# Performance work log

Hardware: AMD Instinct MI355X
Metric: run time of the kernel (lower is better)

## Reference

```python
import jax, jax.numpy as jnp
import numpy as np
import math

B, T, C, H = 8, 1024, 1024, 16
D = C // H  # head dim = 64
EPS = 1e-5


def layernorm(x, g, b):
    mu = jnp.mean(x, axis=-1, keepdims=True)
    var = jnp.var(x, axis=-1, keepdims=True)
    return (x - mu) * jax.lax.rsqrt(var + EPS) * g + b


def setup_inputs() -> dict:
    key = jax.random.key(0)
    ks = jax.random.split(key, 8)
    s = lambda fan_in: 1.0 / math.sqrt(fan_in)
    return {
        "x": jax.random.normal(ks[0], (B, T, C), jnp.float32),
        "Wqkv": jax.random.normal(ks[1], (C, 3 * C), jnp.float32) * s(C),
        "bqkv": jnp.zeros((3 * C,), jnp.float32),
        "Wproj": jax.random.normal(ks[2], (C, C), jnp.float32) * s(C),
        "bproj": jnp.zeros((C,), jnp.float32),
        "ln1_g": jnp.ones((C,), jnp.float32),
        "ln1_b": jnp.zeros((C,), jnp.float32),
        "ln2_g": jnp.ones((C,), jnp.float32),
        "ln2_b": jnp.zeros((C,), jnp.float32),
        "W1": jax.random.normal(ks[3], (C, 4 * C), jnp.float32) * s(C),
        "b1": jnp.zeros((4 * C,), jnp.float32),
        "W2": jax.random.normal(ks[4], (4 * C, C), jnp.float32) * s(4 * C),
        "b2": jnp.zeros((C,), jnp.float32),
    }


def reference(x, Wqkv, bqkv, Wproj, bproj, ln1_g, ln1_b, ln2_g, ln2_b, W1, b1, W2, b2):
    # --- self-attention on ln1(x) ---
    h = layernorm(x, ln1_g, ln1_b)
    qkv = h @ Wqkv + bqkv                          # [B,T,3C]
    q, k, v = jnp.split(qkv, 3, axis=-1)
    # [B,T,C] -> [B,H,T,D]
    q = q.reshape(B, T, H, D).transpose(0, 2, 1, 3)
    k = k.reshape(B, T, H, D).transpose(0, 2, 1, 3)
    v = v.reshape(B, T, H, D).transpose(0, 2, 1, 3)
    # NOTE: original uses 1/sqrt(3*n_embd//n_head), not 1/sqrt(head_dim)
    scale = 1.0 / math.sqrt(3 * C // H)
    attn = jnp.einsum("bhqd,bhkd->bhqk", q, k) * scale  # [B,H,T,T]
    causal = jnp.tril(jnp.ones((T, T), bool))
    attn = jnp.where(causal, attn, -jnp.inf)
    attn = jax.nn.softmax(attn, axis=-1)
    y = jnp.einsum("bhqk,bhkd->bhqd", attn, v)          # [B,H,T,D]
    y = y.transpose(0, 2, 1, 3).reshape(B, T, C)
    x = x + (y @ Wproj + bproj)
    # --- MLP on ln2(x) ---
    h2 = layernorm(x, ln2_g, ln2_b)
    x = x + (jax.nn.relu(h2 @ W1 + b1) @ W2 + b2)
    return x
```

## Files before the change

kernel.cpp:

```cpp
#include <hip/hip_runtime.h>

typedef __bf16 bf16;
typedef __bf16 bf16x8 __attribute__((ext_vector_type(8)));
typedef float f32x4 __attribute__((ext_vector_type(4)));

#define MFMA16(a, b, c) __builtin_amdgcn_mfma_f32_16x16x32_bf16(a, b, c, 0, 0, 0)

static constexpr int Bn = 8;
static constexpr int Tn = 1024;
static constexpr int Cn = 1024;
static constexpr int Hn = 16;

typedef const __attribute__((address_space(1))) unsigned int* gp_t;
typedef __attribute__((address_space(3))) unsigned int* lp_t;
__device__ __forceinline__ void gload_lds16(const bf16* g, bf16* l) {
    __builtin_amdgcn_global_load_lds((gp_t)(const void*)g, (lp_t)(void*)l, 16, 0, 0);
}

__global__ __launch_bounds__(256) void tcast(const float* __restrict__ in,
                                             bf16* __restrict__ out,
                                             int K, int N) {
    __shared__ float tile[32][33];
    const int n0 = blockIdx.x * 32, k0 = blockIdx.y * 32;
    const int tx = threadIdx.x & 31, ty = threadIdx.x >> 5;
#pragma unroll
    for (int i = 0; i < 4; i++)
        tile[ty + 8 * i][tx] = in[(size_t)(k0 + ty + 8 * i) * N + n0 + tx];
    __syncthreads();
#pragma unroll
    for (int i = 0; i < 4; i++)
        out[(size_t)(n0 + ty + 8 * i) * K + k0 + tx] = (bf16)tile[tx][ty + 8 * i];
}

template <typename T>
__global__ __launch_bounds__(256) void ln_row(const T* __restrict__ x,
                                              const float* __restrict__ g,
                                              const float* __restrict__ be,
                                              bf16* __restrict__ out) {
    const int row = blockIdx.x, t = threadIdx.x;
    const T* xr = x + (size_t)row * Cn;
    float v[4], s = 0.f, s2 = 0.f;
#pragma unroll
    for (int i = 0; i < 4; i++) {
        v[i] = (float)xr[t + i * 256];
        s += v[i];
        s2 += v[i] * v[i];
    }
#pragma unroll
    for (int off = 32; off > 0; off >>= 1) {
        s += __shfl_down(s, off);
        s2 += __shfl_down(s2, off);
    }
    __shared__ float red[8];
    const int wave = t >> 6, lane = t & 63;
    if (lane == 0) {
        red[wave] = s;
        red[4 + wave] = s2;
    }
    __syncthreads();
    s = red[0] + red[1] + red[2] + red[3];
    s2 = red[4] + red[5] + red[6] + red[7];
    const float mu = s * (1.f / Cn);
    const float rstd = rsqrtf(s2 * (1.f / Cn) - mu * mu + 1e-5f);
    bf16* orow = out + (size_t)row * Cn;
#pragma unroll
    for (int i = 0; i < 4; i++) {
        int c = t + i * 256;
        orow[c] = (bf16)((v[i] - mu) * rstd * g[c] + be[c]);
    }
}

__global__ __launch_bounds__(256) void vtrans(const bf16* __restrict__ qkv,
                                              bf16* __restrict__ Vt) {
    __shared__ bf16 tile[64 * 72];
    const int tid = threadIdx.x;
    const int bh = blockIdx.x, b = bh >> 4, h = bh & 15;
    const int t0 = blockIdx.y * 64;
    const int r = tid >> 3, c = (tid & 7) * 8;
#pragma unroll
    for (int i = 0; i < 2; i++) {
        const int rr = r + i * 32;
        *(bf16x8*)(tile + rr * 72 + c) =
            *(const bf16x8*)(qkv + ((size_t)(b * Tn + t0 + rr)) * 3072 + 2 * Cn + h * 64 + c);
    }
    __syncthreads();
#pragma unroll
    for (int i = 0; i < 2; i++) {
        const int d = r + i * 32;
        bf16x8 v;
#pragma unroll
        for (int j = 0; j < 8; j++) v[j] = tile[(c + j) * 72 + d];
        *(bf16x8*)(Vt + ((size_t)bh * 64 + d) * Tn + t0 + c) = v;
    }
}

template <int TM, int TN, bool RELU, bool RESID, bool OUTBF16, typename RT>
__global__ __launch_bounds__(256, 2) void gemm_bt(const bf16* __restrict__ A,
                                                  const bf16* __restrict__ Bt,
                                                  const float* __restrict__ bias,
                                                  const RT* __restrict__ resid,
                                                  void* __restrict__ outp,
                                                  int M, int N, int K) {
    constexpr int MI = TM / 32;
    constexpr int NI = TN / 32;
    constexpr int AJ = TM / 32;
    constexpr int BJ = TN / 32;
    __shared__ __align__(16) bf16 As[TM * 64];
    __shared__ __align__(16) bf16 Bs[TN * 64];
    const int t = threadIdx.x;
    const int lane = t & 63, wave = t >> 6;
    const int lane15 = lane & 15, quad = lane >> 4;
    const int m0 = blockIdx.x * TM, n0 = blockIdx.y * TN;
    const int mb = (wave >> 1) * (TM / 2), nb = (wave & 1) * (TN / 2);

    const f32x4 zero4 = {0.f, 0.f, 0.f, 0.f};
    f32x4 acc[MI][NI];
#pragma unroll
    for (int i = 0; i < MI; i++)
#pragma unroll
        for (int j = 0; j < NI; j++) acc[i][j] = zero4;

    const int grow = lane >> 3;
    const int gcol = ((lane & 7) ^ grow) * 8;
    const bf16* gA = A + (size_t)(m0 + wave * (AJ * 8) + grow) * K + gcol;
    const bf16* gB = Bt + (size_t)(n0 + wave * (BJ * 8) + grow) * K + gcol;
    bf16* lA = As + (wave * AJ) * 512;
    bf16* lB = Bs + (wave * BJ) * 512;

    for (int kt = 0; kt < K; kt += 64) {
#pragma unroll
        for (int j = 0; j < AJ; j++)
            gload_lds16(gA + (size_t)(j * 8) * K + kt, lA + j * 512);
#pragma unroll
        for (int j = 0; j < BJ; j++)
            gload_lds16(gB + (size_t)(j * 8) * K + kt, lB + j * 512);
        __syncthreads();
#pragma unroll
        for (int kk = 0; kk < 2; kk++) {
            bf16x8 fa[MI], fb[NI];
#pragma unroll
            for (int mi = 0; mi < MI; mi++) {
                const int r = mb + mi * 16 + lane15;
                fa[mi] = *(const bf16x8*)(As + r * 64 + (((kk * 4 + quad) ^ (r & 7)) * 8));
            }
#pragma unroll
            for (int ni = 0; ni < NI; ni++) {
                const int r = nb + ni * 16 + lane15;
                fb[ni] = *(const bf16x8*)(Bs + r * 64 + (((kk * 4 + quad) ^ (r & 7)) * 8));
            }
#pragma unroll
            for (int mi = 0; mi < MI; mi++)
#pragma unroll
                for (int ni = 0; ni < NI; ni++)
                    acc[mi][ni] = MFMA16(fa[mi], fb[ni], acc[mi][ni]);
        }
        __syncthreads();
    }

    float bsv[NI];
#pragma unroll
    for (int ni = 0; ni < NI; ni++) bsv[ni] = bias[n0 + nb + ni * 16 + lane15];
#pragma unroll
    for (int mi = 0; mi < MI; mi++) {
#pragma unroll
        for (int reg = 0; reg < 4; reg++) {
            const int row = m0 + mb + mi * 16 + quad * 4 + reg;
#pragma unroll
            for (int ni = 0; ni < NI; ni++) {
                const int col = n0 + nb + ni * 16 + lane15;
                float v = acc[mi][ni][reg] + bsv[ni];
                if (RELU) v = v > 0.f ? v : 0.f;
                if (RESID) v += (float)resid[(size_t)row * N + col];
                if (OUTBF16)
                    ((bf16*)outp)[(size_t)row * N + col] = (bf16)v;
                else
                    ((float*)outp)[(size_t)row * N + col] = v;
            }
        }
    }
}

__global__ __launch_bounds__(256) void attn(const bf16* __restrict__ qkv,
                                            const bf16* __restrict__ Vt,
                                            bf16* __restrict__ y) {
    __shared__ __align__(16) bf16 Ks[64 * 72];
    __shared__ __align__(16) bf16 Vs[80 * 72];
    __shared__ __align__(16) bf16 Ps[4][32 * 72];
    const int tid = threadIdx.x, lane = tid & 63, wave = tid >> 6;
    const int lane15 = lane & 15, quad = lane >> 4;
    const int b = blockIdx.x >> 4, h = blockIdx.x & 15;
    const int q0 = blockIdx.y * 128;
    const int qr0 = q0 + wave * 32;
    const float c1 = 0.10412043f;

    for (int i = tid; i < 16 * 72; i += 256)
        Vs[64 * 72 + i] = (bf16)((i < 72) ? 1.0f : 0.0f);

    bf16x8 fq[2][2];
#pragma unroll
    for (int mi = 0; mi < 2; mi++) {
        const size_t qb = ((size_t)(b * Tn + qr0 + mi * 16 + lane15)) * 3072 + h * 64;
#pragma unroll
        for (int kk = 0; kk < 2; kk++)
            fq[mi][kk] = *(const bf16x8*)(qkv + qb + kk * 32 + quad * 8);
    }

    const f32x4 zero4 = {0.f, 0.f, 0.f, 0.f};
    f32x4 o[2][4], lacc[2];
#pragma unroll
    for (int mi = 0; mi < 2; mi++) {
        lacc[mi] = zero4;
#pragma unroll
        for (int ni = 0; ni < 4; ni++) o[mi][ni] = zero4;
    }

    const int sr = tid >> 3, sc = (tid & 7) * 8;
    const int nkb = q0 / 64 + 2;
    for (int kb = 0; kb < nkb; kb++) {
        const int k0 = kb * 64;
#pragma unroll
        for (int i = 0; i < 2; i++) {
            const int r = sr + i * 32;
            *(bf16x8*)(Ks + r * 72 + sc) =
                *(const bf16x8*)(qkv + ((size_t)(b * Tn + k0 + r)) * 3072 + Cn + h * 64 + sc);
            *(bf16x8*)(Vs + r * 72 + sc) =
                *(const bf16x8*)(Vt + ((size_t)blockIdx.x * 64 + r) * Tn + k0 + sc);
        }
        __syncthreads();

        if (k0 <= qr0 + 31) {
            bf16x8 fk[4][2];
#pragma unroll
            for (int ni = 0; ni < 4; ni++)
#pragma unroll
                for (int kk = 0; kk < 2; kk++)
                    fk[ni][kk] = *(const bf16x8*)(Ks + (ni * 16 + lane15) * 72 + kk * 32 + quad * 8);
            f32x4 s[2][4];
#pragma unroll
            for (int mi = 0; mi < 2; mi++)
#pragma unroll
                for (int ni = 0; ni < 4; ni++) {
                    if (k0 + ni * 16 <= qr0 + mi * 16 + 15) {
                        f32x4 a = zero4;
                        a = MFMA16(fq[mi][0], fk[ni][0], a);
                        a = MFMA16(fq[mi][1], fk[ni][1], a);
                        s[mi][ni] = a;
                    }
                }
            const bool domask = (k0 + 63 > qr0);
            if (domask) {
#pragma unroll
                for (int mi = 0; mi < 2; mi++)
#pragma unroll
                    for (int ni = 0; ni < 4; ni++) {
                        bf16* pd = &Ps[wave][(mi * 16 + quad * 4) * 72 + ni * 16 + lane15];
                        if (k0 + ni * 16 > qr0 + mi * 16 + 15) {
#pragma unroll
                            for (int r = 0; r < 4; r++) pd[r * 72] = (bf16)0.f;
                        } else if (k0 + ni * 16 + 15 <= qr0 + mi * 16) {
#pragma unroll
                            for (int r = 0; r < 4; r++)
                                pd[r * 72] = (bf16)__builtin_amdgcn_exp2f(s[mi][ni][r] * c1);
                        } else {
                            const int key = k0 + ni * 16 + lane15;
                            const int row0 = qr0 + mi * 16 + quad * 4;
#pragma unroll
                            for (int r = 0; r < 4; r++) {
                                float L = (key > row0 + r) ? -1e30f : s[mi][ni][r] * c1;
                                pd[r * 72] = (bf16)__builtin_amdgcn_exp2f(L);
                            }
                        }
                    }
            } else {
#pragma unroll
                for (int mi = 0; mi < 2; mi++)
#pragma unroll
                    for (int ni = 0; ni < 4; ni++)
#pragma unroll
                        for (int r = 0; r < 4; r++)
                            Ps[wave][(mi * 16 + quad * 4 + r) * 72 + ni * 16 + lane15] =
                                (bf16)__builtin_amdgcn_exp2f(s[mi][ni][r] * c1);
            }
            bf16x8 fp[2][2];
#pragma unroll
            for (int mi = 0; mi < 2; mi++)
#pragma unroll
                for (int kk = 0; kk < 2; kk++)
                    fp[mi][kk] = *(const bf16x8*)(&Ps[wave][(mi * 16 + lane15) * 72 + kk * 32 + quad * 8]);
            const bool use_kk1 = (k0 + 32 <= qr0 + 31);
#pragma unroll
            for (int ni = 0; ni < 5; ni++) {
                bf16x8 fv0 = *(const bf16x8*)(Vs + (ni * 16 + lane15) * 72 + quad * 8);
                bf16x8 fv1 = *(const bf16x8*)(Vs + (ni * 16 + lane15) * 72 + 32 + quad * 8);
#pragma unroll
                for (int mi = 0; mi < 2; mi++) {
                    f32x4* dst = (ni < 4) ? &o[mi][ni] : &lacc[mi];
                    f32x4 a = *dst;
                    a = MFMA16(fp[mi][0], fv0, a);
                    if (use_kk1) a = MFMA16(fp[mi][1], fv1, a);
                    *dst = a;
                }
            }
        }
        __syncthreads();
    }

#pragma unroll
    for (int mi = 0; mi < 2; mi++)
#pragma unroll
        for (int r = 0; r < 4; r++) {
            float l = __shfl(lacc[mi][r], lane & 48);
            const float inv = 1.f / l;
            const size_t base = ((size_t)(b * Tn + qr0 + mi * 16 + quad * 4 + r)) * Cn + h * 64;
#pragma unroll
            for (int ni = 0; ni < 4; ni++)
                y[base + ni * 16 + lane15] = (bf16)(o[mi][ni][r] * inv);
        }
}

extern "C" void kernel_launch(void* const* d_in, const int* in_sizes, int n_in,
                              void* d_out, int out_size, void* d_ws, size_t ws_size,
                              hipStream_t stream) {
    const float* x = (const float*)d_in[0];
    const float* Wqkv = (const float*)d_in[1];
    const float* bqkv = (const float*)d_in[2];
    const float* Wproj = (const float*)d_in[3];
    const float* bproj = (const float*)d_in[4];
    const float* ln1g = (const float*)d_in[5];
    const float* ln1b = (const float*)d_in[6];
    const float* ln2g = (const float*)d_in[7];
    const float* ln2b = (const float*)d_in[8];
    const float* W1 = (const float*)d_in[9];
    const float* b1 = (const float*)d_in[10];
    const float* W2 = (const float*)d_in[11];
    const float* b2 = (const float*)d_in[12];
    float* out = (float*)d_out;

    char* ws = (char*)d_ws;
    size_t off = 0;
    auto alloc = [&](size_t bytes) {
        void* p = ws + off;
        off += (bytes + 255) & ~(size_t)255;
        return p;
    };
    bf16* WqkvT = (bf16*)alloc((size_t)3072 * 1024 * 2);
    bf16* WprojT = (bf16*)alloc((size_t)1024 * 1024 * 2);
    bf16* W1T = (bf16*)alloc((size_t)4096 * 1024 * 2);
    bf16* W2T = (bf16*)alloc((size_t)1024 * 4096 * 2);
    bf16* hbuf = (bf16*)alloc((size_t)8192 * 1024 * 2);
    bf16* qkvb = (bf16*)alloc((size_t)8192 * 3072 * 2);
    bf16* ybuf = (bf16*)alloc((size_t)8192 * 1024 * 2);
    bf16* vtb = (bf16*)alloc((size_t)8192 * 1024 * 2);
    bf16* x1b = (bf16*)alloc((size_t)8192 * 1024 * 2);
    bf16* a1 = qkvb;

    tcast<<<dim3(3072 / 32, 1024 / 32), 256, 0, stream>>>(Wqkv, WqkvT, 1024, 3072);
    tcast<<<dim3(1024 / 32, 1024 / 32), 256, 0, stream>>>(Wproj, WprojT, 1024, 1024);
    tcast<<<dim3(4096 / 32, 1024 / 32), 256, 0, stream>>>(W1, W1T, 1024, 4096);
    tcast<<<dim3(1024 / 32, 4096 / 32), 256, 0, stream>>>(W2, W2T, 4096, 1024);

    ln_row<float><<<8192, 256, 0, stream>>>(x, ln1g, ln1b, hbuf);
    gemm_bt<128, 256, false, false, true, float><<<dim3(64, 12), 256, 0, stream>>>(
        hbuf, WqkvT, bqkv, (const float*)nullptr, qkvb, 8192, 3072, 1024);
    vtrans<<<dim3(Bn * Hn, Tn / 64), 256, 0, stream>>>(qkvb, vtb);
    attn<<<dim3(Bn * Hn, Tn / 128), 256, 0, stream>>>(qkvb, vtb, ybuf);
    gemm_bt<128, 128, false, true, true, float><<<dim3(64, 8), 256, 0, stream>>>(
        ybuf, WprojT, bproj, x, x1b, 8192, 1024, 1024);
    ln_row<bf16><<<8192, 256, 0, stream>>>(x1b, ln2g, ln2b, hbuf);
    gemm_bt<128, 256, true, false, true, float><<<dim3(64, 16), 256, 0, stream>>>(
        hbuf, W1T, b1, (const float*)nullptr, a1, 8192, 4096, 1024);
    gemm_bt<128, 128, false, true, false, bf16><<<dim3(64, 8), 256, 0, stream>>>(
        a1, W2T, b2, x1b, out, 8192, 1024, 4096);
}
```

Measured before the change: 435.4 us.

## Double-buffer attention K/V via async LDS loads, add BK knob, fuse weight casts

The attention kernel now stages K and V tiles with global_load_lds into double-buffered, XOR-swizzled shared memory. The next block's load is issued before the current block is computed, and the trailing barrier is removed. The P tile also uses the swizzle instead of padding, and the ones-row used for row sums moves to its own buffer. Separately, the GEMM takes a BK template parameter, set to 128 for the two K-heavy N=1024 GEMMs, and the four weight transpose-cast launches are merged into one launch. The intent is to overlap memory with compute and cut launch and barrier overhead. The costs are more LDS, which may lower occupancy, and a possible race on the buffer reuse now that only one barrier remains per iteration.

```diff
diff --git a/kernel.cpp b/kernel.cpp
--- a/kernel.cpp
+++ b/kernel.cpp
@@ -17,11 +17,30 @@
     __builtin_amdgcn_global_load_lds((gp_t)(const void*)g, (lp_t)(void*)l, 16, 0, 0);
 }
 
-__global__ __launch_bounds__(256) void tcast(const float* __restrict__ in,
-                                             bf16* __restrict__ out,
-                                             int K, int N) {
+__global__ __launch_bounds__(256) void tcast_all(const float* __restrict__ Wqkv,
+                                                 const float* __restrict__ Wproj,
+                                                 const float* __restrict__ W1,
+                                                 const float* __restrict__ W2,
+                                                 bf16* __restrict__ WqkvT,
+                                                 bf16* __restrict__ WprojT,
+                                                 bf16* __restrict__ W1T,
+                                                 bf16* __restrict__ W2T) {
+    int bid = blockIdx.x;
+    const float* in;
+    bf16* out;
+    int K, N;
+    if (bid < 3072) {
+        in = Wqkv; out = WqkvT; K = 1024; N = 3072;
+    } else if (bid < 4096) {
+        bid -= 3072; in = Wproj; out = WprojT; K = 1024; N = 1024;
+    } else if (bid < 8192) {
+        bid -= 4096; in = W1; out = W1T; K = 1024; N = 4096;
+    } else {
+        bid -= 8192; in = W2; out = W2T; K = 4096; N = 1024;
+    }
+    const int ntx = N / 32;
+    const int n0 = (bid % ntx) * 32, k0 = (bid / ntx) * 32;
     __shared__ float tile[32][33];
-    const int n0 = blockIdx.x * 32, k0 = blockIdx.y * 32;
     const int tx = threadIdx.x & 31, ty = threadIdx.x >> 5;
 #pragma unroll
     for (int i = 0; i < 4; i++)
@@ -94,7 +113,7 @@
     }
 }
 
-template <int TM, int TN, bool RELU, bool RESID, bool OUTBF16, typename RT>
+template <int TM, int TN, int BK, bool RELU, bool RESID, bool OUTBF16, typename RT>
 __global__ __launch_bounds__(256, 2) void gemm_bt(const bf16* __restrict__ A,
                                                   const bf16* __restrict__ Bt,
                                                   const float* __restrict__ bias,
@@ -103,10 +122,12 @@
                                                   int M, int N, int K) {
     constexpr int MI = TM / 32;
     constexpr int NI = TN / 32;
-    constexpr int AJ = TM / 32;
-    constexpr int BJ = TN / 32;
-    __shared__ __align__(16) bf16 As[TM * 64];
-    __shared__ __align__(16) bf16 Bs[TN * 64];
+    constexpr int CPR = BK / 8;
+    constexpr int RPG = 64 / CPR;
+    constexpr int AJ = TM / (4 * RPG);
+    constexpr int BJ = TN / (4 * RPG);
+    __shared__ __align__(16) bf16 As[TM * BK];
+    __shared__ __align__(16) bf16 Bs[TN * BK];
     const int t = threadIdx.x;
     const int lane = t & 63, wave = t >> 6;
     const int lane15 = lane & 15, quad = lane >> 4;
@@ -120,33 +141,37 @@
 #pragma unroll
         for (int j = 0; j < NI; j++) acc[i][j] = zero4;
 
-    const int grow = lane >> 3;
-    const int gcol = ((lane & 7) ^ grow) * 8;
-    const bf16* gA = A + (size_t)(m0 + wave * (AJ * 8) + grow) * K + gcol;
-    const bf16* gB = Bt + (size_t)(n0 + wave * (BJ * 8) + grow) * K + gcol;
-    bf16* lA = As + (wave * AJ) * 512;
-    bf16* lB = Bs + (wave * BJ) * 512;
-
-    for (int kt = 0; kt < K; kt += 64) {
-#pragma unroll
-        for (int j = 0; j < AJ; j++)
-            gload_lds16(gA + (size_t)(j * 8) * K + kt, lA + j * 512);
-#pragma unroll
-        for (int j = 0; j < BJ; j++)
-            gload_lds16(gB + (size_t)(j * 8) * K + kt, lB + j * 512);
+    const int grow = lane / CPR;
+    const int gsub = lane % CPR;
+
+    for (int kt = 0; kt < K; kt += BK) {
+#pragma unroll
+        for (int j = 0; j < AJ; j++) {
+            const int rj = wave * (AJ * RPG) + j * RPG + grow;
+            const int cj = (gsub ^ (rj & 7)) * 8;
+            gload_lds16(A + (size_t)(m0 + rj) * K + kt + cj,
+                        As + (wave * (AJ * RPG) + j * RPG) * BK);
+        }
+#pragma unroll
+        for (int j = 0; j < BJ; j++) {
+            const int rj = wave * (BJ * RPG) + j * RPG + grow;
+            const int cj = (gsub ^ (rj & 7)) * 8;
+            gload_lds16(Bt + (size_t)(n0 + rj) * K + kt + cj,
+                        Bs + (wave * (BJ * RPG) + j * RPG) * BK);
+        }
         __syncthreads();
 #pragma unroll
-        for (int kk = 0; kk < 2; kk++) {
+        for (int kk = 0; kk < BK / 32; kk++) {
             bf16x8 fa[MI], fb[NI];
 #pragma unroll
             for (int mi = 0; mi < MI; mi++) {
                 const int r = mb + mi * 16 + lane15;
-                fa[mi] = *(const bf16x8*)(As + r * 64 + (((kk * 4 + quad) ^ (r & 7)) * 8));
+                fa[mi] = *(const bf16x8*)(As + r * BK + (((kk * 4 + quad) ^ (r & 7)) * 8));
             }
 #pragma unroll
             for (int ni = 0; ni < NI; ni++) {
                 const int r = nb + ni * 16 + lane15;
-                fb[ni] = *(const bf16x8*)(Bs + r * 64 + (((kk * 4 + quad) ^ (r & 7)) * 8));
+                fb[ni] = *(const bf16x8*)(Bs + r * BK + (((kk * 4 + quad) ^ (r & 7)) * 8));
             }
 #pragma unroll
             for (int mi = 0; mi < MI; mi++)
@@ -183,9 +208,10 @@
 __global__ __launch_bounds__(256) void attn(const bf16* __restrict__ qkv,
                                             const bf16* __restrict__ Vt,
                                             bf16* __restrict__ y) {
-    __shared__ __align__(16) bf16 Ks[64 * 72];
-    __shared__ __align__(16) bf16 Vs[80 * 72];
-    __shared__ __align__(16) bf16 Ps[4][32 * 72];
+    __shared__ __align__(16) bf16 Ks[2][64 * 64];
+    __shared__ __align__(16) bf16 Vs[2][64 * 64];
+    __shared__ __align__(16) bf16 Ones[16 * 64];
+    __shared__ __align__(16) bf16 Ps[4][32 * 64];
     const int tid = threadIdx.x, lane = tid & 63, wave = tid >> 6;
     const int lane15 = lane & 15, quad = lane >> 4;
     const int b = blockIdx.x >> 4, h = blockIdx.x & 15;
@@ -193,8 +219,22 @@
     const int qr0 = q0 + wave * 32;
     const float c1 = 0.10412043f;
 
-    for (int i = tid; i < 16 * 72; i += 256)
-        Vs[64 * 72 + i] = (bf16)((i < 72) ? 1.0f : 0.0f);
+    for (int i = tid; i < 16 * 64; i += 256) Ones[i] = (bf16)((i < 64) ? 1.0f : 0.0f);
+
+    const int grow = lane >> 3;
+    const int gcol = ((lane & 7) ^ grow) * 8;
+    const int srow = wave * 16 + grow;
+    const bf16* gK = qkv + ((size_t)(b * Tn + srow)) * 3072 + Cn + h * 64 + gcol;
+    const bf16* gV = Vt + ((size_t)(blockIdx.x * 64 + srow)) * Tn + gcol;
+
+    auto stage = [&](int kb, int p) {
+        const int k0 = kb * 64;
+#pragma unroll
+        for (int j = 0; j < 2; j++) {
+            gload_lds16(gK + (size_t)(k0 + j * 8) * 3072, &Ks[p][(wave * 16 + j * 8) * 64]);
+            gload_lds16(gV + (size_t)(j * 8) * Tn + k0, &Vs[p][(wave * 16 + j * 8) * 64]);
+        }
+    };
 
     bf16x8 fq[2][2];
 #pragma unroll
@@ -214,27 +254,23 @@
         for (int ni = 0; ni < 4; ni++) o[mi][ni] = zero4;
     }
 
-    const int sr = tid >> 3, sc = (tid & 7) * 8;
+    stage(0, 0);
     const int nkb = q0 / 64 + 2;
     for (int kb = 0; kb < nkb; kb++) {
+        const int p = kb & 1;
         const int k0 = kb * 64;
-#pragma unroll
-        for (int i = 0; i < 2; i++) {
-            const int r = sr + i * 32;
-            *(bf16x8*)(Ks + r * 72 + sc) =
-                *(const bf16x8*)(qkv + ((size_t)(b * Tn + k0 + r)) * 3072 + Cn + h * 64 + sc);
-            *(bf16x8*)(Vs + r * 72 + sc) =
-                *(const bf16x8*)(Vt + ((size_t)blockIdx.x * 64 + r) * Tn + k0 + sc);
-        }
         __syncthreads();
+        if (kb + 1 < nkb) stage(kb + 1, 1 - p);
 
         if (k0 <= qr0 + 31) {
             bf16x8 fk[4][2];
 #pragma unroll
-            for (int ni = 0; ni < 4; ni++)
+            for (int ni = 0; ni < 4; ni++) {
+                const int r = ni * 16 + lane15;
 #pragma unroll
                 for (int kk = 0; kk < 2; kk++)
-                    fk[ni][kk] = *(const bf16x8*)(Ks + (ni * 16 + lane15) * 72 + kk * 32 + quad * 8);
+                    fk[ni][kk] = *(const bf16x8*)(&Ks[p][r * 64 + (((kk * 4 + quad) ^ (r & 7)) * 8)]);
+            }
             f32x4 s[2][4];
 #pragma unroll
             for (int mi = 0; mi < 2; mi++)
@@ -248,50 +284,50 @@
                     }
                 }
             const bool domask = (k0 + 63 > qr0);
-            if (domask) {
-#pragma unroll
-                for (int mi = 0; mi < 2; mi++)
-#pragma unroll
-                    for (int ni = 0; ni < 4; ni++) {
-                        bf16* pd = &Ps[wave][(mi * 16 + quad * 4) * 72 + ni * 16 + lane15];
-                        if (k0 + ni * 16 > qr0 + mi * 16 + 15) {
-#pragma unroll
-                            for (int r = 0; r < 4; r++) pd[r * 72] = (bf16)0.f;
-                        } else if (k0 + ni * 16 + 15 <= qr0 + mi * 16) {
-#pragma unroll
-                            for (int r = 0; r < 4; r++)
-                                pd[r * 72] = (bf16)__builtin_amdgcn_exp2f(s[mi][ni][r] * c1);
+#pragma unroll
+            for (int mi = 0; mi < 2; mi++)
+#pragma unroll
+                for (int ni = 0; ni < 4; ni++) {
+#pragma unroll
+                    for (int r = 0; r < 4; r++) {
+                        const int prow = mi * 16 + quad * 4 + r;
+                        const int r7 = (quad * 4 + r) & 7;
+                        const int paddr = prow * 64 + (((ni * 2 + (lane15 >> 3)) ^ r7) * 8) +
+                                          (lane15 & 7);
+                        float val;
+                        if (domask && (k0 + ni * 16 > qr0 + mi * 16 + 15)) {
+                            val = 0.f;
+                        } else if (domask && (k0 + ni * 16 + 15 > qr0 + mi * 16)) {
+                            const int key = k0 + ni * 16 + lane15;
+                            const int row = qr0 + prow;
+                            float L = (key > row) ? -1e30f : s[mi][ni][r] * c1;
+                            val = __builtin_amdgcn_exp2f(L);
                         } else {
-                            const int key = k0 + ni * 16 + lane15;
-                            const int row0 = qr0 + mi * 16 + quad * 4;
-#pragma unroll
-                            for (int r = 0; r < 4; r++) {
-                                float L = (key > row0 + r) ? -1e30f : s[mi][ni][r] * c1;
-                                pd[r * 72] = (bf16)__builtin_amdgcn_exp2f(L);
-                            }
+                            val = __builtin_amdgcn_exp2f(s[mi][ni][r] * c1);
                         }
+                        Ps[wave][paddr] = (bf16)val;
                     }
-            } else {
-#pragma unroll
-                for (int mi = 0; mi < 2; mi++)
-#pragma unroll
-                    for (int ni = 0; ni < 4; ni++)
-#pragma unroll
-                        for (int r = 0; r < 4; r++)
-                            Ps[wave][(mi * 16 + quad * 4 + r) * 72 + ni * 16 + lane15] =
-                                (bf16)__builtin_amdgcn_exp2f(s[mi][ni][r] * c1);
-            }
+                }
             bf16x8 fp[2][2];
 #pragma unroll
-            for (int mi = 0; mi < 2; mi++)
+            for (int mi = 0; mi < 2; mi++) {
+                const int r = mi * 16 + lane15;
 #pragma unroll
                 for (int kk = 0; kk < 2; kk++)
-                    fp[mi][kk] = *(const bf16x8*)(&Ps[wave][(mi * 16 + lane15) * 72 + kk * 32 + quad * 8]);
+                    fp[mi][kk] = *(const bf16x8*)(&Ps[wave][r * 64 + (((kk * 4 + quad) ^ (r & 7)) * 8)]);
+            }
             const bool use_kk1 = (k0 + 32 <= qr0 + 31);
 #pragma unroll
             for (int ni = 0; ni < 5; ni++) {
-                bf16x8 fv0 = *(const bf16x8*)(Vs + (ni * 16 + lane15) * 72 + quad * 8);
-                bf16x8 fv1 = *(const bf16x8*)(Vs + (ni * 16 + lane15) * 72 + 32 + quad * 8);
+                bf16x8 fv0, fv1;
+                if (ni < 4) {
+                    const int r = ni * 16 + lane15;
+                    fv0 = *(const bf16x8*)(&Vs[p][r * 64 + ((quad ^ (r & 7)) * 8)]);
+                    fv1 = *(const bf16x8*)(&Vs[p][r * 64 + (((4 + quad) ^ (r & 7)) * 8)]);
+                } else {
+                    fv0 = *(const bf16x8*)(Ones + lane15 * 64 + quad * 8);
+                    fv1 = *(const bf16x8*)(Ones + lane15 * 64 + 32 + quad * 8);
+                }
 #pragma unroll
                 for (int mi = 0; mi < 2; mi++) {
                     f32x4* dst = (ni < 4) ? &o[mi][ni] : &lacc[mi];
@@ -302,7 +338,6 @@
                 }
             }
         }
-        __syncthreads();
     }
 
 #pragma unroll
@@ -354,21 +389,18 @@
     bf16* x1b = (bf16*)alloc((size_t)8192 * 1024 * 2);
     bf16* a1 = qkvb;
 
-    tcast<<<dim3(3072 / 32, 1024 / 32), 256, 0, stream>>>(Wqkv, WqkvT, 1024, 3072);
-    tcast<<<dim3(1024 / 32, 1024 / 32), 256, 0, stream>>>(Wproj, WprojT, 1024, 1024);
-    tcast<<<dim3(4096 / 32, 1024 / 32), 256, 0, stream>>>(W1, W1T, 1024, 4096);
-    tcast<<<dim3(1024 / 32, 4096 / 32), 256, 0, stream>>>(W2, W2T, 4096, 1024);
+    tcast_all<<<12288, 256, 0, stream>>>(Wqkv, Wproj, W1, W2, WqkvT, WprojT, W1T, W2T);
 
     ln_row<float><<<8192, 256, 0, stream>>>(x, ln1g, ln1b, hbuf);
-    gemm_bt<128, 256, false, false, true, float><<<dim3(64, 12), 256, 0, stream>>>(
+    gemm_bt<128, 256, 64, false, false, true, float><<<dim3(64, 12), 256, 0, stream>>>(
         hbuf, WqkvT, bqkv, (const float*)nullptr, qkvb, 8192, 3072, 1024);
     vtrans<<<dim3(Bn * Hn, Tn / 64), 256, 0, stream>>>(qkvb, vtb);
     attn<<<dim3(Bn * Hn, Tn / 128), 256, 0, stream>>>(qkvb, vtb, ybuf);
-    gemm_bt<128, 128, false, true, true, float><<<dim3(64, 8), 256, 0, stream>>>(
+    gemm_bt<128, 128, 128, false, true, true, float><<<dim3(64, 8), 256, 0, stream>>>(
         ybuf, WprojT, bproj, x, x1b, 8192, 1024, 1024);
     ln_row<bf16><<<8192, 256, 0, stream>>>(x1b, ln2g, ln2b, hbuf);
-    gemm_bt<128, 256, true, false, true, float><<<dim3(64, 16), 256, 0, stream>>>(
+    gemm_bt<128, 256, 64, true, false, true, float><<<dim3(64, 16), 256, 0, stream>>>(
         hbuf, W1T, b1, (const float*)nullptr, a1, 8192, 4096, 1024);
-    gemm_bt<128, 128, false, true, false, bf16><<<dim3(64, 8), 256, 0, stream>>>(
+    gemm_bt<128, 128, 128, false, true, false, bf16><<<dim3(64, 8), 256, 0, stream>>>(
         a1, W2T, b2, x1b, out, 8192, 1024, 4096);
 }
```

Measured after the change: 440.4 us. About the same (+1.1%).
